# Performance work log

Measured on AMD Instinct MI355X. Metric: run time of the kernel, lower is better.

Reference implementation:

```python
import jax, jax.numpy as jnp
import numpy as np

DEPTH = 7  # complete binary trees with 2**DEPTH = 128 leaves

B, L = 4096, 128
V, E, OUT = 100000, 128, 3


def setup_inputs() -> dict:
    key = jax.random.key(0)
    ks = jax.random.split(key, 6)
    tokens = jax.random.randint(ks[0], (B, L), 0, V, dtype=jnp.int64)
    embedding = jax.random.normal(ks[1], (V, E), dtype=jnp.float32)
    # tree_layer: Linear(2E -> E); torch stores weight as [out, in]
    W_tree = jax.random.normal(ks[2], (E, 2 * E), dtype=jnp.float32) * (1.0 / np.sqrt(2 * E))
    b_tree = jax.random.normal(ks[3], (E,), dtype=jnp.float32) * 0.01
    # classifier_layer: Linear(E -> OUT)
    W_cls = jax.random.normal(ks[4], (OUT, E), dtype=jnp.float32) * (1.0 / np.sqrt(E))
    b_cls = jax.random.normal(ks[5], (OUT,), dtype=jnp.float32) * 0.01
    return {"tokens": tokens, "embedding": embedding, "W_tree": W_tree,
            "b_tree": b_tree, "W_cls": W_cls, "b_cls": b_cls}


def reference(tokens, embedding, W_tree, b_tree, W_cls, b_cls):
    # Leaf embeddings: gather rows of the embedding table. [B, L, E]
    reps = embedding[tokens]
    # Level-synchronous bottom-up composition (depth-batched across all trees):
    # at each level, pair adjacent nodes, concat features, apply tree_layer + tanh.
    for _ in range(DEPTH):
        left = reps[:, 0::2, :]   # [B, n/2, E]
        right = reps[:, 1::2, :]  # [B, n/2, E]
        combined = jnp.concatenate([left, right], axis=-1)  # [B, n/2, 2E]
        reps = jnp.tanh(jnp.einsum('bnh,eh->bne', combined, W_tree) + b_tree)
    roots = reps[:, 0, :]  # [B, E]
    return roots @ W_cls.T + b_cls  # [B, OUT]
```

## Files before the change

kernel.cpp:

```cpp
#include <hip/hip_runtime.h>
#include <hip/hip_fp16.h>


typedef _Float16 half8 __attribute__((ext_vector_type(8)));
typedef float floatx4 __attribute__((ext_vector_type(4)));

#define STRIDE 264
#define NSAMP 4096

__device__ __forceinline__ float fast_tanh(float x) {
  float e = __expf(2.f * x);
  return 1.f - 2.f * __builtin_amdgcn_rcpf(e + 1.f);
}

__device__ __forceinline__ unsigned pkrtz(float a, float b) {
  auto h = __builtin_amdgcn_cvt_pkrtz(a, b);
  return __builtin_bit_cast(unsigned, h);
}

template<int MT, int MOUT, bool ROOT>
__device__ __forceinline__ void level_run(
    const _Float16* inb, _Float16* outb, float* rootbuf,
    const half8 (&Wf)[2][8], const float (&bias)[2],
    int nbase, int l15, int quad)
{
  floatx4 acc[MT][2];

  if (MT == 1) {
    floatx4 accB[2];
    acc[0][0] = (floatx4){0.f, 0.f, 0.f, 0.f};
    acc[0][1] = (floatx4){0.f, 0.f, 0.f, 0.f};
    accB[0]   = (floatx4){0.f, 0.f, 0.f, 0.f};
    accB[1]   = (floatx4){0.f, 0.f, 0.f, 0.f};
    const _Float16* arow = inb + l15 * STRIDE + quad * 8;
#pragma unroll
    for (int ks = 0; ks < 4; ++ks) {
      half8 a0 = *(const half8*)(arow + ks * 32);
      half8 a1 = *(const half8*)(arow + (ks + 4) * 32);
      acc[0][0] = __builtin_amdgcn_mfma_f32_16x16x32_f16(a0, Wf[0][ks],     acc[0][0], 0, 0, 0);
      accB[0]   = __builtin_amdgcn_mfma_f32_16x16x32_f16(a1, Wf[0][ks + 4], accB[0],   0, 0, 0);
      acc[0][1] = __builtin_amdgcn_mfma_f32_16x16x32_f16(a0, Wf[1][ks],     acc[0][1], 0, 0, 0);
      accB[1]   = __builtin_amdgcn_mfma_f32_16x16x32_f16(a1, Wf[1][ks + 4], accB[1],   0, 0, 0);
    }
    acc[0][0] += accB[0];
    acc[0][1] += accB[1];
  } else {
#pragma unroll
    for (int m = 0; m < MT; ++m) {
      acc[m][0] = (floatx4){0.f, 0.f, 0.f, 0.f};
      acc[m][1] = (floatx4){0.f, 0.f, 0.f, 0.f};
    }
#pragma unroll
    for (int m = 0; m < MT; ++m) {
      const _Float16* arow = inb + (m * 16 + l15) * STRIDE + quad * 8;
#pragma unroll
      for (int ks = 0; ks < 8; ++ks) {
        half8 a = *(const half8*)(arow + ks * 32);
        acc[m][0] = __builtin_amdgcn_mfma_f32_16x16x32_f16(a, Wf[0][ks], acc[m][0], 0, 0, 0);
        acc[m][1] = __builtin_amdgcn_mfma_f32_16x16x32_f16(a, Wf[1][ks], acc[m][1], 0, 0, 0);
      }
    }
  }

  const int mrow = quad * 4;
#pragma unroll
  for (int m = 0; m < MT; ++m) {
#pragma unroll
    for (int i = 0; i < 2; ++i) {
      const int col = (nbase + i) * 16 + l15;
      const float b = bias[i];
#pragma unroll
      for (int r = 0; r < 4; ++r) {
        const int node = m * 16 + mrow + r;
        if (node < MOUT) {
          float v = fast_tanh(acc[m][i][r] + b);
          if (ROOT) {
            rootbuf[col] = v;
          } else {
            outb[(node >> 1) * STRIDE + (node & 1) * 128 + col] = (_Float16)v;
          }
        }
      }
    }
  }
}

__global__ __launch_bounds__(256, 3)
void tree_kernel(const int* __restrict__ tokens,
                 const float* __restrict__ embedding,
                 const float* __restrict__ W_tree,
                 const float* __restrict__ b_tree,
                 const float* __restrict__ W_cls,
                 const float* __restrict__ b_cls,
                 float* __restrict__ out)
{
  __shared__ __align__(16) _Float16 bufA[64 * STRIDE];
  __shared__ __align__(16) _Float16 bufB[32 * STRIDE];
  __shared__ float rootbuf[128];

  const int tid  = threadIdx.x;
  const int wid  = tid >> 6;
  const int lane = tid & 63;
  const int l15  = lane & 15;
  const int quad = lane >> 4;
  const int nbase = wid * 2;

  half8 Wf[2][8];
#pragma unroll
  for (int i = 0; i < 2; ++i) {
    const int e = (nbase + i) * 16 + l15;
#pragma unroll
    for (int ks = 0; ks < 8; ++ks) {
      const int k = ks * 32 + quad * 8;
      const float4* p = (const float4*)(W_tree + e * 256 + k);
      float4 lo = p[0], hi = p[1];
      half8 f;
      f[0] = (_Float16)lo.x; f[1] = (_Float16)lo.y; f[2] = (_Float16)lo.z; f[3] = (_Float16)lo.w;
      f[4] = (_Float16)hi.x; f[5] = (_Float16)hi.y; f[6] = (_Float16)hi.z; f[7] = (_Float16)hi.w;
      Wf[i][ks] = f;
    }
  }
  float bias[2];
#pragma unroll
  for (int i = 0; i < 2; ++i) bias[i] = b_tree[(nbase + i) * 16 + l15];

  const int leaf = tid >> 1;
  const int hh   = tid & 1;

#pragma unroll 1
  for (int s = blockIdx.x; s < NSAMP; s += gridDim.x) {

    {
      const int tok = tokens[s * 128 + leaf];
      const float4* src = (const float4*)(embedding + (size_t)tok * 128 + hh * 64);
      uint4* dst = (uint4*)bufA + (leaf >> 1) * 33 + (leaf & 1) * 16 + hh * 8;
#pragma unroll
      for (int j = 0; j < 8; ++j) {
        float4 x = src[2 * j], y = src[2 * j + 1];
        uint4 w;
        w.x = pkrtz(x.x, x.y); w.y = pkrtz(x.z, x.w);
        w.z = pkrtz(y.x, y.y); w.w = pkrtz(y.z, y.w);
        dst[j] = w;
      }
    }
    __syncthreads();

    level_run<4, 64, false>(bufA, bufB, rootbuf, Wf, bias, nbase, l15, quad);
    __syncthreads();
    level_run<2, 32, false>(bufB, bufA, rootbuf, Wf, bias, nbase, l15, quad);
    __syncthreads();
    level_run<1, 16, false>(bufA, bufB, rootbuf, Wf, bias, nbase, l15, quad);
    __syncthreads();
    level_run<1,  8, false>(bufB, bufA, rootbuf, Wf, bias, nbase, l15, quad);
    __syncthreads();
    level_run<1,  4, false>(bufA, bufB, rootbuf, Wf, bias, nbase, l15, quad);
    __syncthreads();
    level_run<1,  2, false>(bufB, bufA, rootbuf, Wf, bias, nbase, l15, quad);
    __syncthreads();
    level_run<1,  1, true >(bufA, bufB, rootbuf, Wf, bias, nbase, l15, quad);
    __syncthreads();

    if (wid == 0) {
      const float r0 = rootbuf[lane];
      const float r1 = rootbuf[lane + 64];
#pragma unroll
      for (int o = 0; o < 3; ++o) {
        float p = r0 * W_cls[o * 128 + lane] + r1 * W_cls[o * 128 + 64 + lane];
#pragma unroll
        for (int sh = 32; sh > 0; sh >>= 1) p += __shfl_down(p, sh, 64);
        if (lane == 0) out[s * 3 + o] = p + b_cls[o];
      }
    }
  }
}

extern "C" void kernel_launch(void* const* d_in, const int* in_sizes, int n_in,
                              void* d_out, int out_size, void* d_ws, size_t ws_size,
                              hipStream_t stream) {
  const int*   tokens    = (const int*)d_in[0];
  const float* embedding = (const float*)d_in[1];
  const float* W_tree    = (const float*)d_in[2];
  const float* b_tree    = (const float*)d_in[3];
  const float* W_cls     = (const float*)d_in[4];
  const float* b_cls     = (const float*)d_in[5];
  float* out = (float*)d_out;

  dim3 grid(768), block(256);
  tree_kernel<<<grid, block, 0, stream>>>(tokens, embedding, W_tree, b_tree, W_cls, b_cls, out);
}
```

Before: 164.0 us.

## Batch two samples' upper tree levels together and fuse classifier into root level

Each block now processes pairs of samples. The lower five levels run per sample, and the last two levels of both samples are merged into shared MFMA passes, so the near-empty 16-row tiles of the tiny top levels are issued half as often. The classifier is fused into the root epilogue: each wave keeps its W_cls slice in registers, reduces its partial dot products with shuffles and writes them to shared memory, and six threads finish the sum. This removes two barriers and one MFMA level per sample and drops the separate wave-0 classifier pass. In exchange the grid has only 2048 pairs of work, which may leave some CUs with uneven load.

```diff
diff --git a/kernel.cpp b/kernel.cpp
--- a/kernel.cpp
+++ b/kernel.cpp
@@ -6,7 +6,7 @@
 typedef float floatx4 __attribute__((ext_vector_type(4)));
 
 #define STRIDE 264
-#define NSAMP 4096
+#define NPAIR 2048
 
 __device__ __forceinline__ float fast_tanh(float x) {
   float e = __expf(2.f * x);
@@ -18,32 +18,35 @@
   return __builtin_bit_cast(unsigned, h);
 }
 
-template<int MT, int MOUT, bool ROOT>
-__device__ __forceinline__ void level_run(
-    const _Float16* inb, _Float16* outb, float* rootbuf,
+__device__ __forceinline__ void mfma_k256(const _Float16* arow, const half8 (&Wf)[2][8],
+                                          floatx4 (&accO)[2]) {
+  floatx4 aA[2], aB[2];
+  aA[0] = (floatx4){0.f, 0.f, 0.f, 0.f}; aA[1] = (floatx4){0.f, 0.f, 0.f, 0.f};
+  aB[0] = (floatx4){0.f, 0.f, 0.f, 0.f}; aB[1] = (floatx4){0.f, 0.f, 0.f, 0.f};
+#pragma unroll
+  for (int ks = 0; ks < 4; ++ks) {
+    half8 x0 = *(const half8*)(arow + ks * 32);
+    half8 x1 = *(const half8*)(arow + (ks + 4) * 32);
+    aA[0] = __builtin_amdgcn_mfma_f32_16x16x32_f16(x0, Wf[0][ks],     aA[0], 0, 0, 0);
+    aB[0] = __builtin_amdgcn_mfma_f32_16x16x32_f16(x1, Wf[0][ks + 4], aB[0], 0, 0, 0);
+    aA[1] = __builtin_amdgcn_mfma_f32_16x16x32_f16(x0, Wf[1][ks],     aA[1], 0, 0, 0);
+    aB[1] = __builtin_amdgcn_mfma_f32_16x16x32_f16(x1, Wf[1][ks + 4], aB[1], 0, 0, 0);
+  }
+  accO[0] = aA[0] + aB[0];
+  accO[1] = aA[1] + aB[1];
+}
+
+template<int MT, int MOUT>
+__device__ __forceinline__ void level_std(
+    const _Float16* inb, _Float16* outb,
     const half8 (&Wf)[2][8], const float (&bias)[2],
     int nbase, int l15, int quad)
 {
   floatx4 acc[MT][2];
-
   if (MT == 1) {
-    floatx4 accB[2];
-    acc[0][0] = (floatx4){0.f, 0.f, 0.f, 0.f};
-    acc[0][1] = (floatx4){0.f, 0.f, 0.f, 0.f};
-    accB[0]   = (floatx4){0.f, 0.f, 0.f, 0.f};
-    accB[1]   = (floatx4){0.f, 0.f, 0.f, 0.f};
-    const _Float16* arow = inb + l15 * STRIDE + quad * 8;
-#pragma unroll
-    for (int ks = 0; ks < 4; ++ks) {
-      half8 a0 = *(const half8*)(arow + ks * 32);
-      half8 a1 = *(const half8*)(arow + (ks + 4) * 32);
-      acc[0][0] = __builtin_amdgcn_mfma_f32_16x16x32_f16(a0, Wf[0][ks],     acc[0][0], 0, 0, 0);
-      accB[0]   = __builtin_amdgcn_mfma_f32_16x16x32_f16(a1, Wf[0][ks + 4], accB[0],   0, 0, 0);
-      acc[0][1] = __builtin_amdgcn_mfma_f32_16x16x32_f16(a0, Wf[1][ks],     acc[0][1], 0, 0, 0);
-      accB[1]   = __builtin_amdgcn_mfma_f32_16x16x32_f16(a1, Wf[1][ks + 4], accB[1],   0, 0, 0);
-    }
-    acc[0][0] += accB[0];
-    acc[0][1] += accB[1];
+    floatx4 a2[2];
+    mfma_k256(inb + l15 * STRIDE + quad * 8, Wf, a2);
+    acc[0][0] = a2[0]; acc[0][1] = a2[1];
   } else {
 #pragma unroll
     for (int m = 0; m < MT; ++m) {
@@ -74,11 +77,7 @@
         const int node = m * 16 + mrow + r;
         if (node < MOUT) {
           float v = fast_tanh(acc[m][i][r] + b);
-          if (ROOT) {
-            rootbuf[col] = v;
-          } else {
-            outb[(node >> 1) * STRIDE + (node & 1) * 128 + col] = (_Float16)v;
-          }
+          outb[(node >> 1) * STRIDE + (node & 1) * 128 + col] = (_Float16)v;
         }
       }
     }
@@ -96,7 +95,8 @@
 {
   __shared__ __align__(16) _Float16 bufA[64 * STRIDE];
   __shared__ __align__(16) _Float16 bufB[32 * STRIDE];
-  __shared__ float rootbuf[128];
+  __shared__ __align__(16) _Float16 bufC[4 * STRIDE];
+  __shared__ float wavepart[4][2][3];
 
   const int tid  = threadIdx.x;
   const int wid  = tid >> 6;
@@ -124,52 +124,104 @@
 #pragma unroll
   for (int i = 0; i < 2; ++i) bias[i] = b_tree[(nbase + i) * 16 + l15];
 
+  float wc[2][3];
+#pragma unroll
+  for (int i = 0; i < 2; ++i) {
+    const int col = (nbase + i) * 16 + l15;
+#pragma unroll
+    for (int o = 0; o < 3; ++o) wc[i][o] = W_cls[o * 128 + col];
+  }
+
   const int leaf = tid >> 1;
   const int hh   = tid & 1;
 
 #pragma unroll 1
-  for (int s = blockIdx.x; s < NSAMP; s += gridDim.x) {
+  for (int p = blockIdx.x; p < NPAIR; p += gridDim.x) {
+
+#pragma unroll 1
+    for (int j = 0; j < 2; ++j) {
+      const int s = 2 * p + j;
+      {
+        const int tok = tokens[s * 128 + leaf];
+        const float4* src = (const float4*)(embedding + (size_t)tok * 128 + hh * 64);
+        uint4* dst = (uint4*)bufA + (leaf >> 1) * 33 + (leaf & 1) * 16 + hh * 8;
+#pragma unroll
+        for (int jj = 0; jj < 8; ++jj) {
+          float4 x = src[2 * jj], y = src[2 * jj + 1];
+          uint4 w;
+          w.x = pkrtz(x.x, x.y); w.y = pkrtz(x.z, x.w);
+          w.z = pkrtz(y.x, y.y); w.w = pkrtz(y.z, y.w);
+          dst[jj] = w;
+        }
+      }
+      __syncthreads();
+      level_std<4, 64>(bufA, bufB, Wf, bias, nbase, l15, quad);
+      __syncthreads();
+      level_std<2, 32>(bufB, bufA, Wf, bias, nbase, l15, quad);
+      __syncthreads();
+      level_std<1, 16>(bufA, bufB, Wf, bias, nbase, l15, quad);
+      __syncthreads();
+      level_std<1,  8>(bufB, bufA, Wf, bias, nbase, l15, quad);
+      __syncthreads();
+      level_std<1,  4>(bufA, bufC + j * 2 * STRIDE,
+                       Wf, bias, nbase, l15, quad);
+      __syncthreads();
+    }
 
     {
-      const int tok = tokens[s * 128 + leaf];
-      const float4* src = (const float4*)(embedding + (size_t)tok * 128 + hh * 64);
-      uint4* dst = (uint4*)bufA + (leaf >> 1) * 33 + (leaf & 1) * 16 + hh * 8;
-#pragma unroll
-      for (int j = 0; j < 8; ++j) {
-        float4 x = src[2 * j], y = src[2 * j + 1];
-        uint4 w;
-        w.x = pkrtz(x.x, x.y); w.y = pkrtz(x.z, x.w);
-        w.z = pkrtz(y.x, y.y); w.w = pkrtz(y.z, y.w);
-        dst[j] = w;
+      const int rclamp = l15 < 4 ? l15 : 3;
+      floatx4 acc[2];
+      mfma_k256(bufC + rclamp * STRIDE + quad * 8, Wf, acc);
+      const int mrow = quad * 4;
+#pragma unroll
+      for (int i = 0; i < 2; ++i) {
+        const int col = (nbase + i) * 16 + l15;
+#pragma unroll
+        for (int r = 0; r < 4; ++r) {
+          const int mr = mrow + r;
+          if (mr < 4) {
+            float v = fast_tanh(acc[i][r] + bias[i]);
+            bufA[(mr >> 1) * STRIDE + (mr & 1) * 128 + col] = (_Float16)v;
+          }
+        }
       }
     }
     __syncthreads();
 
-    level_run<4, 64, false>(bufA, bufB, rootbuf, Wf, bias, nbase, l15, quad);
+    {
+      floatx4 acc[2];
+      mfma_k256(bufA + l15 * STRIDE + quad * 8, Wf, acc);
+      float part[2][3] = {{0.f, 0.f, 0.f}, {0.f, 0.f, 0.f}};
+      if (quad == 0) {
+#pragma unroll
+        for (int i = 0; i < 2; ++i) {
+#pragma unroll
+          for (int rr = 0; rr < 2; ++rr) {
+            float v = fast_tanh(acc[i][rr] + bias[i]);
+#pragma unroll
+            for (int o = 0; o < 3; ++o) part[rr][o] = fmaf(v, wc[i][o], part[rr][o]);
+          }
+        }
+      }
+#pragma unroll
+      for (int rr = 0; rr < 2; ++rr) {
+#pragma unroll
+        for (int o = 0; o < 3; ++o) {
+          float v = part[rr][o];
+          v += __shfl_down(v, 8);
+          v += __shfl_down(v, 4);
+          v += __shfl_down(v, 2);
+          v += __shfl_down(v, 1);
+          if (lane == 0) wavepart[wid][rr][o] = v;
+        }
+      }
+    }
     __syncthreads();
-    level_run<2, 32, false>(bufB, bufA, rootbuf, Wf, bias, nbase, l15, quad);
-    __syncthreads();
-    level_run<1, 16, false>(bufA, bufB, rootbuf, Wf, bias, nbase, l15, quad);
-    __syncthreads();
-    level_run<1,  8, false>(bufB, bufA, rootbuf, Wf, bias, nbase, l15, quad);
-    __syncthreads();
-    level_run<1,  4, false>(bufA, bufB, rootbuf, Wf, bias, nbase, l15, quad);
-    __syncthreads();
-    level_run<1,  2, false>(bufB, bufA, rootbuf, Wf, bias, nbase, l15, quad);
-    __syncthreads();
-    level_run<1,  1, true >(bufA, bufB, rootbuf, Wf, bias, nbase, l15, quad);
-    __syncthreads();
-
-    if (wid == 0) {
-      const float r0 = rootbuf[lane];
-      const float r1 = rootbuf[lane + 64];
-#pragma unroll
-      for (int o = 0; o < 3; ++o) {
-        float p = r0 * W_cls[o * 128 + lane] + r1 * W_cls[o * 128 + 64 + lane];
-#pragma unroll
-        for (int sh = 32; sh > 0; sh >>= 1) p += __shfl_down(p, sh, 64);
-        if (lane == 0) out[s * 3 + o] = p + b_cls[o];
-      }
+    if (tid < 6) {
+      const int rr = tid / 3, o = tid - 3 * rr;
+      float v = wavepart[0][rr][o] + wavepart[1][rr][o]
+              + wavepart[2][rr][o] + wavepart[3][rr][o];
+      out[(2 * p + rr) * 3 + o] = v + b_cls[o];
     }
   }
 }
```

Measured after the change: 156.8 us. 1.05x faster.
